# Performance work log

Hardware: AMD Instinct MI355X
Metric: run time of the kernel (lower is better)

Reference implementation:

```python
import jax, jax.numpy as jnp
import numpy as np

B, N, E, C_IN, C_OUT = 16, 4096, 131072, 256, 256


def setup_inputs() -> dict:
    key = jax.random.key(0)
    k1, k2, k3, k4 = jax.random.split(key, 4)
    x = jax.random.normal(k1, (B, N, C_IN), dtype=jnp.float32)
    edge_index = jax.random.randint(k2, (B, 2, E), 0, N, dtype=jnp.int32)
    edge_weight = jax.random.uniform(k3, (B, E), dtype=jnp.float32)
    # glorot init for weight [C_in, C_out]
    scale = float(np.sqrt(6.0 / (C_IN + C_OUT)))
    W = jax.random.uniform(k4, (C_IN, C_OUT), dtype=jnp.float32, minval=-scale, maxval=scale)
    return {"x": x, "edge_index": edge_index, "edge_weight": edge_weight, "W": W}


def _gcn_one_graph(xi, ei, ewi, W):
    # xi: [N, C_in], ei: [2, E+N], ewi: [E+N]
    n = xi.shape[0]
    row, col = ei[0], ei[1]
    deg = jax.ops.segment_sum(ewi, row, num_segments=n)            # [N]
    deg_inv = jnp.where(deg > 0, jax.lax.rsqrt(deg), 0.0)          # deg^-0.5, inf -> 0
    norm = deg_inv[row] * ewi * deg_inv[col]                       # [E+N]
    xw = xi @ W                                                    # [N, C_out]
    msg = norm[:, None] * xw[col]                                  # gather + scale
    out = jax.ops.segment_sum(msg, row, num_segments=n)            # scatter-add to rows
    return jax.nn.relu(out)                                        # act = F.relu, bias=False


def reference(x, edge_index, edge_weight, W):
    b, n, _ = x.shape
    # add self loops with weight 1 (fill_value=1)
    loop = jnp.arange(n, dtype=edge_index.dtype)
    loop_idx = jnp.broadcast_to(jnp.stack([loop, loop])[None], (b, 2, n))
    ei = jnp.concatenate([edge_index, loop_idx], axis=-1)          # [B, 2, E+N]
    ew = jnp.concatenate([edge_weight, jnp.ones((b, n), x.dtype)], axis=-1)  # [B, E+N]
    return jax.vmap(_gcn_one_graph, in_axes=(0, 0, 0, None))(x, ei, ew, W)
```

## Files before the change

### kernel.cpp

```cpp
#include <hip/hip_runtime.h>
#include <cstdint>
#include <cstddef>

#define BB 16
#define NN 4096
#define EE 131072
#define CIN 256
#define COUT 256
#define NCH 16
#define CHE (EE / NCH)

typedef __attribute__((ext_vector_type(8))) __bf16 bf16x8;
typedef __attribute__((ext_vector_type(4))) float f32x4;
typedef __attribute__((ext_vector_type(2))) float f32x2;

#define GLDS16(g, l) __builtin_amdgcn_global_load_lds( \
    (const __attribute__((address_space(1))) uint32_t*)(g), \
    (__attribute__((address_space(3))) uint32_t*)(l), 16, 0, 0)

__global__ __launch_bounds__(256) void cvt_wt_kernel(const float* __restrict__ W, __bf16* __restrict__ wt) {
    int n = blockIdx.x;
    int k = threadIdx.x;
    wt[n * CIN + k] = (__bf16)W[(size_t)k * COUT + n];
}

__global__ __launch_bounds__(256) void phaseA_kernel(const float* __restrict__ x, __bf16* __restrict__ xbf,
                                                     const int* __restrict__ ei, const float* __restrict__ ew,
                                                     int* __restrict__ chist, float* __restrict__ wdeg) {
    __shared__ int h[NN];
    __shared__ float wh[NN];
    int bid = blockIdx.x;
    int tid = threadIdx.x;
    if (bid < BB * NCH) {
        int b = bid >> 4, c = bid & (NCH - 1);
        for (int i = tid; i < NN; i += 256) { h[i] = 0; wh[i] = 0.f; }
        __syncthreads();
        const int* rows = ei + (size_t)b * 2 * EE + (size_t)c * CHE;
        const float* w = ew + (size_t)b * EE + (size_t)c * CHE;
        #pragma unroll 4
        for (int j = 0; j < CHE / 256; ++j) {
            int row = rows[j * 256 + tid];
            float wv = w[j * 256 + tid];
            atomicAdd(&h[row], 1);
            atomicAdd(&wh[row], wv);
        }
        __syncthreads();
        int* co = chist + ((size_t)b * NCH + c) * NN;
        float* wo = wdeg + ((size_t)b * NCH + c) * NN;
        for (int i = tid; i < NN; i += 256) { co[i] = h[i]; wo[i] = wh[i]; }
    } else {
        size_t u = (size_t)(bid - BB * NCH) * 256 + tid;
        const float* g = &x[u * 8];
        float4 f0 = *reinterpret_cast<const float4*>(g);
        float4 f1 = *reinterpret_cast<const float4*>(g + 4);
        bf16x8 v;
        v[0] = (__bf16)f0.x; v[1] = (__bf16)f0.y; v[2] = (__bf16)f0.z; v[3] = (__bf16)f0.w;
        v[4] = (__bf16)f1.x; v[5] = (__bf16)f1.y; v[6] = (__bf16)f1.z; v[7] = (__bf16)f1.w;
        *reinterpret_cast<bf16x8*>(&xbf[u * 8]) = v;
    }
}

__global__ __launch_bounds__(1024) void scanfused_kernel(const int* __restrict__ chist, const float* __restrict__ wdeg,
                                                         int* __restrict__ chunkbase, int* __restrict__ roff,
                                                         float* __restrict__ dinv) {
    int b = blockIdx.x, tid = threadIdx.x;
    int wid = tid >> 6, lane = tid & 63;
    __shared__ int wsum[16];
    __shared__ int wbase[16];
    __shared__ int gtot_s;
    int carry = 0;
    for (int g = 0; g < 4; ++g) {
        int r = g * 1024 + tid;
        int cv[NCH];
        int tot = 0;
        float dsum = 1.0f;
        #pragma unroll
        for (int c = 0; c < NCH; ++c) {
            size_t idx = ((size_t)b * NCH + c) * NN + r;
            cv[c] = chist[idx];
            tot += cv[c];
            dsum += wdeg[idx];
        }
        dinv[b * NN + r] = rsqrtf(dsum);
        int incl = tot;
        #pragma unroll
        for (int off = 1; off < 64; off <<= 1) {
            int t = __shfl_up(incl, off, 64);
            if (lane >= off) incl += t;
        }
        if (lane == 63) wsum[wid] = incl;
        __syncthreads();
        if (wid == 0) {
            int v = (lane < 16) ? wsum[lane] : 0;
            int winc = v;
            #pragma unroll
            for (int off = 1; off < 16; off <<= 1) {
                int t = __shfl_up(winc, off, 64);
                if (lane >= off) winc += t;
            }
            if (lane < 16) wbase[lane] = winc - v;
            if (lane == 15) gtot_s = winc;
        }
        __syncthreads();
        int excl = carry + wbase[wid] + (incl - tot);
        roff[b * NN + r] = excl;
        int acc = excl;
        #pragma unroll
        for (int c = 0; c < NCH; ++c) {
            chunkbase[((size_t)b * NCH + c) * NN + r] = acc;
            acc += cv[c];
        }
        carry += gtot_s;
        __syncthreads();
    }
}

__global__ __launch_bounds__(256) void scatter2_kernel(const int* __restrict__ ei, const float* __restrict__ ew,
                                                       const float* __restrict__ dinv, const int* __restrict__ chunkbase,
                                                       int2* __restrict__ csr) {
    __shared__ int basebuf[NN];
    __shared__ float dinvs[NN];
    int bid = blockIdx.x;
    int xcd = bid & 7;
    int j = bid >> 3;
    int b = xcd * 2 + (j >> 4);
    int c = j & (NCH - 1);
    int tid = threadIdx.x;
    for (int i = tid; i < NN; i += 256) {
        basebuf[i] = chunkbase[((size_t)b * NCH + c) * NN + i];
        dinvs[i] = dinv[b * NN + i];
    }
    __syncthreads();
    const int* rows = ei + (size_t)b * 2 * EE + (size_t)c * CHE;
    const int* cols = rows + EE;
    const float* w = ew + (size_t)b * EE + (size_t)c * CHE;
    int2* cs = csr + (size_t)b * EE;
    #pragma unroll 4
    for (int jj = 0; jj < CHE / 256; ++jj) {
        int e = jj * 256 + tid;
        int row = rows[e];
        int col = cols[e];
        float nm = dinvs[row] * w[e] * dinvs[col];
        int pos = atomicAdd(&basebuf[row], 1);
        int2 pk; pk.x = col * (COUT * 2); pk.y = __float_as_int(nm);
        cs[pos] = pk;
    }
}

__global__ __launch_bounds__(256) void gemm_glds_kernel(const __bf16* __restrict__ xbf, const __bf16* __restrict__ wt,
                                                        __bf16* __restrict__ xw) {
    __shared__ __bf16 As[128 * 64];
    __shared__ __bf16 Bs[128 * 64];
    int tid = threadIdx.x;
    int lane = tid & 63;
    int wave = tid >> 6;
    int bx = blockIdx.x >> 1, by = blockIdx.x & 1;
    int row0 = bx * 128, col0 = by * 128;
    int wr = wave >> 1, wc = wave & 1;
    int hi = lane >> 4, lo = lane & 15;
    int lr = lane >> 3, lk = (lane & 7) * 8;
    f32x4 acc[4][4] = {};

    for (int kk = 0; kk < CIN; kk += 64) {
        #pragma unroll
        for (int j = 0; j < 4; ++j) {
            int seg = j * 4 + wave;
            const __bf16* ga = &xbf[(size_t)(row0 + seg * 8 + lr) * CIN + kk + lk];
            const __bf16* gb = &wt [(size_t)(col0 + seg * 8 + lr) * CIN + kk + lk];
            GLDS16(ga, &As[seg * 512]);
            GLDS16(gb, &Bs[seg * 512]);
        }
        __syncthreads();
        #pragma unroll
        for (int ks = 0; ks < 2; ++ks) {
            bf16x8 a[4], b[4];
            #pragma unroll
            for (int m = 0; m < 4; ++m)
                a[m] = *reinterpret_cast<const bf16x8*>(&As[(wr * 64 + m * 16 + lo) * 64 + ks * 32 + 8 * hi]);
            #pragma unroll
            for (int n = 0; n < 4; ++n)
                b[n] = *reinterpret_cast<const bf16x8*>(&Bs[(wc * 64 + n * 16 + lo) * 64 + ks * 32 + 8 * hi]);
            #pragma unroll
            for (int m = 0; m < 4; ++m)
                #pragma unroll
                for (int n = 0; n < 4; ++n)
                    acc[m][n] = __builtin_amdgcn_mfma_f32_16x16x32_bf16(a[m], b[n], acc[m][n], 0, 0, 0);
        }
        __syncthreads();
    }
    #pragma unroll
    for (int m = 0; m < 4; ++m)
        #pragma unroll
        for (int n = 0; n < 4; ++n)
            #pragma unroll
            for (int r = 0; r < 4; ++r) {
                int row = row0 + wr * 64 + m * 16 + hi * 4 + r;
                int col = col0 + wc * 64 + n * 16 + lo;
                xw[(size_t)row * COUT + col] = (__bf16)acc[m][n][r];
            }
}

#define BFLO(u) __uint_as_float((u) << 16)
#define BFHI(u) __uint_as_float((u) & 0xffff0000u)
#define ACC8(nm, raw) { \
    acc0.x += (nm) * BFLO((raw).x); acc0.y += (nm) * BFHI((raw).x); \
    acc1.x += (nm) * BFLO((raw).y); acc1.y += (nm) * BFHI((raw).y); \
    acc2.x += (nm) * BFLO((raw).z); acc2.y += (nm) * BFHI((raw).z); \
    acc3.x += (nm) * BFLO((raw).w); acc3.y += (nm) * BFHI((raw).w); }

__global__ __launch_bounds__(256) void aggregate_kernel(const __bf16* __restrict__ xw, const float* __restrict__ dinv,
                                                        const int* __restrict__ roff, const int2* __restrict__ csr,
                                                        float* __restrict__ out) {
    int bid = blockIdx.x;
    int xcd = bid & 7;
    int idx = bid >> 3;
    int b = xcd * 2 + (idx >> 10);
    int rowblk = idx & 1023;
    int wave = threadIdx.x >> 6;
    int lane = threadIdx.x & 63;
    int n = rowblk * 4 + wave;
    bool hiHalf = lane >= 32;
    int sub = lane & 31;

    const int* rb = roff + b * NN;
    int s = __builtin_amdgcn_readfirstlane(rb[n]);
    int eRaw = (n == NN - 1) ? EE : rb[n + 1];
    int e = __builtin_amdgcn_readfirstlane(eRaw);
    int cnt = e - s;
    const int2* cs = csr + (size_t)b * EE + s;

    const char* xwb = (const char*)(xw + (size_t)b * NN * COUT) + sub * 16;
    f32x2 acc0 = {0.f, 0.f}, acc1 = {0.f, 0.f}, acc2 = {0.f, 0.f}, acc3 = {0.f, 0.f};

    {
        float di = dinv[b * NN + n];
        float sn = hiHalf ? 0.f : di * di;
        uint4 raw = *reinterpret_cast<const uint4*>(xwb + (size_t)n * (COUT * 2));
        ACC8(sn, raw);
    }

    int m = cnt & ~7;
    int i = 0;
    for (; i < m; i += 8) {
        int2 q[8];
        #pragma unroll
        for (int u = 0; u < 8; ++u) q[u] = cs[i + u];
        #pragma unroll
        for (int u = 0; u < 4; ++u) {
            int offx = hiHalf ? q[2 * u + 1].x : q[2 * u].x;
            float nm = __int_as_float(hiHalf ? q[2 * u + 1].y : q[2 * u].y);
            uint4 raw = *reinterpret_cast<const uint4*>(xwb + offx);
            ACC8(nm, raw);
        }
    }
    if (i < cnt) {
        #pragma unroll
        for (int u = 0; u < 4; ++u) {
            int j0 = i + 2 * u, j1 = j0 + 1;
            int jc0 = (j0 < cnt) ? j0 : cnt - 1;
            int jc1 = (j1 < cnt) ? j1 : cnt - 1;
            int2 q0 = cs[jc0];
            int2 q1 = cs[jc1];
            int offx = hiHalf ? q1.x : q0.x;
            float nm0 = (j0 < cnt) ? __int_as_float(q0.y) : 0.f;
            float nm1 = (j1 < cnt) ? __int_as_float(q1.y) : 0.f;
            float nm = hiHalf ? nm1 : nm0;
            uint4 raw = *reinterpret_cast<const uint4*>(xwb + offx);
            ACC8(nm, raw);
        }
    }

    acc0.x += __shfl(acc0.x, lane ^ 32, 64); acc0.y += __shfl(acc0.y, lane ^ 32, 64);
    acc1.x += __shfl(acc1.x, lane ^ 32, 64); acc1.y += __shfl(acc1.y, lane ^ 32, 64);
    acc2.x += __shfl(acc2.x, lane ^ 32, 64); acc2.y += __shfl(acc2.y, lane ^ 32, 64);
    acc3.x += __shfl(acc3.x, lane ^ 32, 64); acc3.y += __shfl(acc3.y, lane ^ 32, 64);

    float4 o = hiHalf
        ? make_float4(fmaxf(acc2.x, 0.f), fmaxf(acc2.y, 0.f), fmaxf(acc3.x, 0.f), fmaxf(acc3.y, 0.f))
        : make_float4(fmaxf(acc0.x, 0.f), fmaxf(acc0.y, 0.f), fmaxf(acc1.x, 0.f), fmaxf(acc1.y, 0.f));
    float* orow = out + ((size_t)b * NN + n) * COUT + sub * 8 + (hiHalf ? 4 : 0);
    *reinterpret_cast<float4*>(orow) = o;
}

__global__ __launch_bounds__(256) void init_deg_kernel(float* __restrict__ deg, float v) {
    int i = blockIdx.x * 256 + threadIdx.x;
    if (i < BB * NN) deg[i] = v;
}

__global__ __launch_bounds__(256) void deg_only_kernel(const int* __restrict__ ei, const float* __restrict__ ew,
                                                       float* __restrict__ deg) {
    int idx = blockIdx.x * 256 + threadIdx.x;
    if (idx >= BB * EE) return;
    int b = idx / EE, e = idx - b * EE;
    atomicAdd(&deg[b * NN + ei[(size_t)b * 2 * EE + e]], ew[(size_t)b * EE + e]);
}

__global__ __launch_bounds__(256) void deginv_kernel(const float* __restrict__ deg, float* __restrict__ dinv) {
    int i = blockIdx.x * 256 + threadIdx.x;
    if (i < BB * NN) {
        float d = deg[i];
        dinv[i] = (d > 0.0f) ? rsqrtf(d) : 0.0f;
    }
}

__global__ __launch_bounds__(256) void gemm_f32src_kernel(const float* __restrict__ x, const __bf16* __restrict__ wt,
                                                          __bf16* __restrict__ xw) {
    __shared__ __bf16 As[128][64];
    __shared__ __bf16 Bs[128][64];
    int tid = threadIdx.x;
    int lane = tid & 63;
    int wave = tid >> 6;
    int row0 = blockIdx.x * 128;
    int col0 = blockIdx.y * 128;
    int wr = wave >> 1, wc = wave & 1;
    int hi = lane >> 4, lo = lane & 15;
    f32x4 acc[4][4] = {};
    for (int kk = 0; kk < CIN; kk += 64) {
        #pragma unroll
        for (int j = 0; j < 4; ++j) {
            int c = j * 256 + tid;
            int r = c >> 3, kq = c & 7;
            const float* g = &x[(size_t)(row0 + r) * CIN + kk + 8 * kq];
            float4 f0 = *reinterpret_cast<const float4*>(g);
            float4 f1 = *reinterpret_cast<const float4*>(g + 4);
            bf16x8 v;
            v[0] = (__bf16)f0.x; v[1] = (__bf16)f0.y; v[2] = (__bf16)f0.z; v[3] = (__bf16)f0.w;
            v[4] = (__bf16)f1.x; v[5] = (__bf16)f1.y; v[6] = (__bf16)f1.z; v[7] = (__bf16)f1.w;
            *reinterpret_cast<bf16x8*>(&As[r][8 * kq]) = v;
        }
        #pragma unroll
        for (int j = 0; j < 4; ++j) {
            int c = j * 256 + tid;
            int r = c >> 3, kq = c & 7;
            *reinterpret_cast<bf16x8*>(&Bs[r][8 * kq]) =
                *reinterpret_cast<const bf16x8*>(&wt[(size_t)(col0 + r) * CIN + kk + 8 * kq]);
        }
        __syncthreads();
        #pragma unroll
        for (int ks = 0; ks < 2; ++ks) {
            bf16x8 a[4], b[4];
            #pragma unroll
            for (int m = 0; m < 4; ++m)
                a[m] = *reinterpret_cast<const bf16x8*>(&As[wr * 64 + m * 16 + lo][ks * 32 + 8 * hi]);
            #pragma unroll
            for (int n = 0; n < 4; ++n)
                b[n] = *reinterpret_cast<const bf16x8*>(&Bs[wc * 64 + n * 16 + lo][ks * 32 + 8 * hi]);
            #pragma unroll
            for (int m = 0; m < 4; ++m)
                #pragma unroll
                for (int n = 0; n < 4; ++n)
                    acc[m][n] = __builtin_amdgcn_mfma_f32_16x16x32_bf16(a[m], b[n], acc[m][n], 0, 0, 0);
        }
        __syncthreads();
    }
    #pragma unroll
    for (int m = 0; m < 4; ++m)
        #pragma unroll
        for (int n = 0; n < 4; ++n)
            #pragma unroll
            for (int r = 0; r < 4; ++r) {
                int row = row0 + wr * 64 + m * 16 + hi * 4 + r;
                int col = col0 + wc * 64 + n * 16 + lo;
                xw[(size_t)row * COUT + col] = (__bf16)acc[m][n][r];
            }
}

__global__ __launch_bounds__(256) void self_kernel(const __bf16* __restrict__ xw, const float* __restrict__ dinv,
                                                   float* __restrict__ out) {
    int bn = blockIdx.x;
    int c = threadIdx.x;
    float di = dinv[bn];
    out[(size_t)bn * COUT + c] = di * di * (float)xw[(size_t)bn * COUT + c];
}

__global__ __launch_bounds__(256) void scatter_atomic_kernel(const int* __restrict__ ei, const float* __restrict__ ew,
                                                             const float* __restrict__ dinv,
                                                             const __bf16* __restrict__ xw, float* __restrict__ out) {
    int be = blockIdx.x;
    int b = be / EE, e = be - b * EE;
    int c = threadIdx.x;
    int row = ei[(size_t)b * 2 * EE + e];
    int col = ei[(size_t)b * 2 * EE + EE + e];
    float w = ew[(size_t)b * EE + e];
    float nm = dinv[b * NN + row] * w * dinv[b * NN + col];
    const __bf16* xwb = xw + (size_t)b * NN * COUT;
    atomicAdd(&out[((size_t)b * NN + row) * COUT + c], nm * (float)xwb[(size_t)col * COUT + c]);
}

__global__ __launch_bounds__(256) void relu_kernel(float* __restrict__ out) {
    size_t i = (size_t)blockIdx.x * 256 + threadIdx.x;
    out[i] = fmaxf(out[i], 0.0f);
}

extern "C" void kernel_launch(void* const* d_in, const int* in_sizes, int n_in,
                              void* d_out, int out_size, void* d_ws, size_t ws_size,
                              hipStream_t stream) {
    const float* x  = (const float*)d_in[0];
    const int*   ei = (const int*)d_in[1];
    const float* ew = (const float*)d_in[2];
    const float* Wm = (const float*)d_in[3];
    float* out = (float*)d_out;

    char* ws = (char*)d_ws;
    size_t off = 0;
    auto alloc = [&](size_t bytes) -> void* {
        void* p = ws + off;
        off += (bytes + 255) & ~(size_t)255;
        return p;
    };
    __bf16* xw        = (__bf16*)alloc((size_t)BB * NN * COUT * 2);
    __bf16* xbf       = (__bf16*)alloc((size_t)BB * NN * CIN * 2);
    int*    chist     = (int*)alloc((size_t)BB * NCH * NN * 4);
    float*  wdeg      = (float*)alloc((size_t)BB * NCH * NN * 4);
    int*    chunkbase = (int*)alloc((size_t)BB * NCH * NN * 4);
    int*    roff      = (int*)alloc((size_t)BB * NN * 4);
    float*  dinv      = (float*)alloc((size_t)BB * NN * 4);
    __bf16* wt        = (__bf16*)alloc((size_t)CIN * COUT * 2);
    int2*   csr       = (int2*)xbf;
    float*  deg_fb    = (float*)chist;
    bool use_csr = (ws_size >= off);

    cvt_wt_kernel<<<COUT, CIN, 0, stream>>>(Wm, wt);

    if (use_csr) {
        phaseA_kernel<<<BB * NCH + (BB * NN * CIN) / (256 * 8), 256, 0, stream>>>(x, xbf, ei, ew, chist, wdeg);
        scanfused_kernel<<<BB, 1024, 0, stream>>>(chist, wdeg, chunkbase, roff, dinv);
        gemm_glds_kernel<<<(BB * NN / 128) * (COUT / 128), 256, 0, stream>>>(xbf, wt, xw);
        scatter2_kernel<<<BB * NCH, 256, 0, stream>>>(ei, ew, dinv, chunkbase, csr);
        aggregate_kernel<<<BB * NN / 4, 256, 0, stream>>>(xw, dinv, roff, csr, out);
    } else {
        const int bnBlocks = (BB * NN) / 256;
        init_deg_kernel<<<bnBlocks, 256, 0, stream>>>(deg_fb, 1.0f);
        deg_only_kernel<<<(BB * EE) / 256, 256, 0, stream>>>(ei, ew, deg_fb);
        deginv_kernel<<<bnBlocks, 256, 0, stream>>>(deg_fb, dinv);
        dim3 ggrid((BB * NN) / 128, COUT / 128);
        gemm_f32src_kernel<<<ggrid, 256, 0, stream>>>(x, wt, xw);
        self_kernel<<<BB * NN, 256, 0, stream>>>(xw, dinv, out);
        scatter_atomic_kernel<<<BB * EE, 256, 0, stream>>>(ei, ew, dinv, xw, out);
        relu_kernel<<<(BB * NN * COUT) / 256, 256, 0, stream>>>(out);
    }
}
```

Before: 140.6 us.

## Switch GEMM and gather path from bf16 to fp16 and fuse weight conversion

Changes the intermediate x, W and xW buffers from bf16 to fp16, using the f16 MFMA and fp16-to-float conversions in the aggregation gather. It also folds the W transpose and convert step into the phaseA kernel as extra blocks, which removes one kernel launch on the CSR path. fp16 gives more mantissa precision but less range; the aggregate loop now converts halves with hardware instructions instead of bf16 shift and mask tricks.

```diff
diff --git a/kernel.cpp b/kernel.cpp
--- a/kernel.cpp
+++ b/kernel.cpp
@@ -10,21 +10,15 @@
 #define NCH 16
 #define CHE (EE / NCH)
 
-typedef __attribute__((ext_vector_type(8))) __bf16 bf16x8;
+typedef __attribute__((ext_vector_type(8))) _Float16 h16x8;
 typedef __attribute__((ext_vector_type(4))) float f32x4;
-typedef __attribute__((ext_vector_type(2))) float f32x2;
 
 #define GLDS16(g, l) __builtin_amdgcn_global_load_lds( \
     (const __attribute__((address_space(1))) uint32_t*)(g), \
     (__attribute__((address_space(3))) uint32_t*)(l), 16, 0, 0)
 
-__global__ __launch_bounds__(256) void cvt_wt_kernel(const float* __restrict__ W, __bf16* __restrict__ wt) {
-    int n = blockIdx.x;
-    int k = threadIdx.x;
-    wt[n * CIN + k] = (__bf16)W[(size_t)k * COUT + n];
-}
-
-__global__ __launch_bounds__(256) void phaseA_kernel(const float* __restrict__ x, __bf16* __restrict__ xbf,
+__global__ __launch_bounds__(256) void phaseA_kernel(const float* __restrict__ x, _Float16* __restrict__ xh,
+                                                     const float* __restrict__ W, _Float16* __restrict__ wt,
                                                      const int* __restrict__ ei, const float* __restrict__ ew,
                                                      int* __restrict__ chist, float* __restrict__ wdeg) {
     __shared__ int h[NN];
@@ -48,15 +42,19 @@
         int* co = chist + ((size_t)b * NCH + c) * NN;
         float* wo = wdeg + ((size_t)b * NCH + c) * NN;
         for (int i = tid; i < NN; i += 256) { co[i] = h[i]; wo[i] = wh[i]; }
-    } else {
+    } else if (bid < BB * NCH + (BB * NN * CIN) / (256 * 8)) {
         size_t u = (size_t)(bid - BB * NCH) * 256 + tid;
         const float* g = &x[u * 8];
         float4 f0 = *reinterpret_cast<const float4*>(g);
         float4 f1 = *reinterpret_cast<const float4*>(g + 4);
-        bf16x8 v;
-        v[0] = (__bf16)f0.x; v[1] = (__bf16)f0.y; v[2] = (__bf16)f0.z; v[3] = (__bf16)f0.w;
-        v[4] = (__bf16)f1.x; v[5] = (__bf16)f1.y; v[6] = (__bf16)f1.z; v[7] = (__bf16)f1.w;
-        *reinterpret_cast<bf16x8*>(&xbf[u * 8]) = v;
+        h16x8 v;
+        v[0] = (_Float16)f0.x; v[1] = (_Float16)f0.y; v[2] = (_Float16)f0.z; v[3] = (_Float16)f0.w;
+        v[4] = (_Float16)f1.x; v[5] = (_Float16)f1.y; v[6] = (_Float16)f1.z; v[7] = (_Float16)f1.w;
+        *reinterpret_cast<h16x8*>(&xh[u * 8]) = v;
+    } else {
+        int n = bid - (BB * NCH + (BB * NN * CIN) / (256 * 8));
+        int k = tid;
+        wt[n * CIN + k] = (_Float16)W[(size_t)k * COUT + n];
     }
 }
 
@@ -115,6 +113,59 @@
     }
 }
 
+__global__ __launch_bounds__(256) void gemm_glds_kernel(const _Float16* __restrict__ xh, const _Float16* __restrict__ wt,
+                                                        _Float16* __restrict__ xw) {
+    __shared__ _Float16 As[128 * 64];
+    __shared__ _Float16 Bs[128 * 64];
+    int tid = threadIdx.x;
+    int lane = tid & 63;
+    int wave = tid >> 6;
+    int bx = blockIdx.x >> 1, by = blockIdx.x & 1;
+    int row0 = bx * 128, col0 = by * 128;
+    int wr = wave >> 1, wc = wave & 1;
+    int hi = lane >> 4, lo = lane & 15;
+    int lr = lane >> 3, lk = (lane & 7) * 8;
+    f32x4 acc[4][4] = {};
+
+    for (int kk = 0; kk < CIN; kk += 64) {
+        #pragma unroll
+        for (int j = 0; j < 4; ++j) {
+            int seg = j * 4 + wave;
+            const _Float16* ga = &xh[(size_t)(row0 + seg * 8 + lr) * CIN + kk + lk];
+            const _Float16* gb = &wt [(size_t)(col0 + seg * 8 + lr) * CIN + kk + lk];
+            GLDS16(ga, &As[seg * 512]);
+            GLDS16(gb, &Bs[seg * 512]);
+        }
+        __syncthreads();
+        #pragma unroll
+        for (int ks = 0; ks < 2; ++ks) {
+            h16x8 a[4], b[4];
+            #pragma unroll
+            for (int m = 0; m < 4; ++m)
+                a[m] = *reinterpret_cast<const h16x8*>(&As[(wr * 64 + m * 16 + lo) * 64 + ks * 32 + 8 * hi]);
+            #pragma unroll
+            for (int n = 0; n < 4; ++n)
+                b[n] = *reinterpret_cast<const h16x8*>(&Bs[(wc * 64 + n * 16 + lo) * 64 + ks * 32 + 8 * hi]);
+            #pragma unroll
+            for (int m = 0; m < 4; ++m)
+                #pragma unroll
+                for (int n = 0; n < 4; ++n)
+                    acc[m][n] = __builtin_amdgcn_mfma_f32_16x16x32_f16(a[m], b[n], acc[m][n], 0, 0, 0);
+        }
+        __syncthreads();
+    }
+    #pragma unroll
+    for (int m = 0; m < 4; ++m)
+        #pragma unroll
+        for (int n = 0; n < 4; ++n)
+            #pragma unroll
+            for (int r = 0; r < 4; ++r) {
+                int row = row0 + wr * 64 + m * 16 + hi * 4 + r;
+                int col = col0 + wc * 64 + n * 16 + lo;
+                xw[(size_t)row * COUT + col] = (_Float16)acc[m][n][r];
+            }
+}
+
 __global__ __launch_bounds__(256) void scatter2_kernel(const int* __restrict__ ei, const float* __restrict__ ew,
                                                        const float* __restrict__ dinv, const int* __restrict__ chunkbase,
                                                        int2* __restrict__ csr) {
@@ -147,68 +198,13 @@
     }
 }
 
-__global__ __launch_bounds__(256) void gemm_glds_kernel(const __bf16* __restrict__ xbf, const __bf16* __restrict__ wt,
-                                                        __bf16* __restrict__ xw) {
-    __shared__ __bf16 As[128 * 64];
-    __shared__ __bf16 Bs[128 * 64];
-    int tid = threadIdx.x;
-    int lane = tid & 63;
-    int wave = tid >> 6;
-    int bx = blockIdx.x >> 1, by = blockIdx.x & 1;
-    int row0 = bx * 128, col0 = by * 128;
-    int wr = wave >> 1, wc = wave & 1;
-    int hi = lane >> 4, lo = lane & 15;
-    int lr = lane >> 3, lk = (lane & 7) * 8;
-    f32x4 acc[4][4] = {};
-
-    for (int kk = 0; kk < CIN; kk += 64) {
-        #pragma unroll
-        for (int j = 0; j < 4; ++j) {
-            int seg = j * 4 + wave;
-            const __bf16* ga = &xbf[(size_t)(row0 + seg * 8 + lr) * CIN + kk + lk];
-            const __bf16* gb = &wt [(size_t)(col0 + seg * 8 + lr) * CIN + kk + lk];
-            GLDS16(ga, &As[seg * 512]);
-            GLDS16(gb, &Bs[seg * 512]);
-        }
-        __syncthreads();
-        #pragma unroll
-        for (int ks = 0; ks < 2; ++ks) {
-            bf16x8 a[4], b[4];
-            #pragma unroll
-            for (int m = 0; m < 4; ++m)
-                a[m] = *reinterpret_cast<const bf16x8*>(&As[(wr * 64 + m * 16 + lo) * 64 + ks * 32 + 8 * hi]);
-            #pragma unroll
-            for (int n = 0; n < 4; ++n)
-                b[n] = *reinterpret_cast<const bf16x8*>(&Bs[(wc * 64 + n * 16 + lo) * 64 + ks * 32 + 8 * hi]);
-            #pragma unroll
-            for (int m = 0; m < 4; ++m)
-                #pragma unroll
-                for (int n = 0; n < 4; ++n)
-                    acc[m][n] = __builtin_amdgcn_mfma_f32_16x16x32_bf16(a[m], b[n], acc[m][n], 0, 0, 0);
-        }
-        __syncthreads();
-    }
-    #pragma unroll
-    for (int m = 0; m < 4; ++m)
-        #pragma unroll
-        for (int n = 0; n < 4; ++n)
-            #pragma unroll
-            for (int r = 0; r < 4; ++r) {
-                int row = row0 + wr * 64 + m * 16 + hi * 4 + r;
-                int col = col0 + wc * 64 + n * 16 + lo;
-                xw[(size_t)row * COUT + col] = (__bf16)acc[m][n][r];
-            }
-}
-
-#define BFLO(u) __uint_as_float((u) << 16)
-#define BFHI(u) __uint_as_float((u) & 0xffff0000u)
-#define ACC8(nm, raw) { \
-    acc0.x += (nm) * BFLO((raw).x); acc0.y += (nm) * BFHI((raw).x); \
-    acc1.x += (nm) * BFLO((raw).y); acc1.y += (nm) * BFHI((raw).y); \
-    acc2.x += (nm) * BFLO((raw).z); acc2.y += (nm) * BFHI((raw).z); \
-    acc3.x += (nm) * BFLO((raw).w); acc3.y += (nm) * BFHI((raw).w); }
-
-__global__ __launch_bounds__(256) void aggregate_kernel(const __bf16* __restrict__ xw, const float* __restrict__ dinv,
+#define ACCH(nm, r) { \
+    a0 += (nm) * (float)(r)[0]; a1 += (nm) * (float)(r)[1]; \
+    a2 += (nm) * (float)(r)[2]; a3 += (nm) * (float)(r)[3]; \
+    a4 += (nm) * (float)(r)[4]; a5 += (nm) * (float)(r)[5]; \
+    a6 += (nm) * (float)(r)[6]; a7 += (nm) * (float)(r)[7]; }
+
+__global__ __launch_bounds__(256) void aggregate_kernel(const _Float16* __restrict__ xw, const float* __restrict__ dinv,
                                                         const int* __restrict__ roff, const int2* __restrict__ csr,
                                                         float* __restrict__ out) {
     int bid = blockIdx.x;
@@ -221,6 +217,7 @@
     int n = rowblk * 4 + wave;
     bool hiHalf = lane >= 32;
     int sub = lane & 31;
+    int lanebyte = sub * 16;
 
     const int* rb = roff + b * NN;
     int s = __builtin_amdgcn_readfirstlane(rb[n]);
@@ -229,14 +226,14 @@
     int cnt = e - s;
     const int2* cs = csr + (size_t)b * EE + s;
 
-    const char* xwb = (const char*)(xw + (size_t)b * NN * COUT) + sub * 16;
-    f32x2 acc0 = {0.f, 0.f}, acc1 = {0.f, 0.f}, acc2 = {0.f, 0.f}, acc3 = {0.f, 0.f};
+    const char* xwbase = (const char*)(xw + (size_t)b * NN * COUT);
+    float a0 = 0.f, a1 = 0.f, a2 = 0.f, a3 = 0.f, a4 = 0.f, a5 = 0.f, a6 = 0.f, a7 = 0.f;
 
     {
         float di = dinv[b * NN + n];
         float sn = hiHalf ? 0.f : di * di;
-        uint4 raw = *reinterpret_cast<const uint4*>(xwb + (size_t)n * (COUT * 2));
-        ACC8(sn, raw);
+        h16x8 r = *reinterpret_cast<const h16x8*>(xwbase + (size_t)n * (COUT * 2) + lanebyte);
+        ACCH(sn, r);
     }
 
     int m = cnt & ~7;
@@ -247,10 +244,10 @@
         for (int u = 0; u < 8; ++u) q[u] = cs[i + u];
         #pragma unroll
         for (int u = 0; u < 4; ++u) {
-            int offx = hiHalf ? q[2 * u + 1].x : q[2 * u].x;
+            int offx = (hiHalf ? q[2 * u + 1].x : q[2 * u].x) + lanebyte;
             float nm = __int_as_float(hiHalf ? q[2 * u + 1].y : q[2 * u].y);
-            uint4 raw = *reinterpret_cast<const uint4*>(xwb + offx);
-            ACC8(nm, raw);
+            h16x8 r = *reinterpret_cast<const h16x8*>(xwbase + (uint32_t)offx);
+            ACCH(nm, r);
         }
     }
     if (i < cnt) {
@@ -261,25 +258,31 @@
             int jc1 = (j1 < cnt) ? j1 : cnt - 1;
             int2 q0 = cs[jc0];
             int2 q1 = cs[jc1];
-            int offx = hiHalf ? q1.x : q0.x;
+            int offx = (hiHalf ? q1.x : q0.x) + lanebyte;
             float nm0 = (j0 < cnt) ? __int_as_float(q0.y) : 0.f;
             float nm1 = (j1 < cnt) ? __int_as_float(q1.y) : 0.f;
             float nm = hiHalf ? nm1 : nm0;
-            uint4 raw = *reinterpret_cast<const uint4*>(xwb + offx);
-            ACC8(nm, raw);
-        }
-    }
-
-    acc0.x += __shfl(acc0.x, lane ^ 32, 64); acc0.y += __shfl(acc0.y, lane ^ 32, 64);
-    acc1.x += __shfl(acc1.x, lane ^ 32, 64); acc1.y += __shfl(acc1.y, lane ^ 32, 64);
-    acc2.x += __shfl(acc2.x, lane ^ 32, 64); acc2.y += __shfl(acc2.y, lane ^ 32, 64);
-    acc3.x += __shfl(acc3.x, lane ^ 32, 64); acc3.y += __shfl(acc3.y, lane ^ 32, 64);
+            h16x8 r = *reinterpret_cast<const h16x8*>(xwbase + (uint32_t)offx);
+            ACCH(nm, r);
+        }
+    }
+
+    a0 += __shfl(a0, lane ^ 32, 64); a1 += __shfl(a1, lane ^ 32, 64);
+    a2 += __shfl(a2, lane ^ 32, 64); a3 += __shfl(a3, lane ^ 32, 64);
+    a4 += __shfl(a4, lane ^ 32, 64); a5 += __shfl(a5, lane ^ 32, 64);
+    a6 += __shfl(a6, lane ^ 32, 64); a7 += __shfl(a7, lane ^ 32, 64);
 
     float4 o = hiHalf
-        ? make_float4(fmaxf(acc2.x, 0.f), fmaxf(acc2.y, 0.f), fmaxf(acc3.x, 0.f), fmaxf(acc3.y, 0.f))
-        : make_float4(fmaxf(acc0.x, 0.f), fmaxf(acc0.y, 0.f), fmaxf(acc1.x, 0.f), fmaxf(acc1.y, 0.f));
+        ? make_float4(fmaxf(a4, 0.f), fmaxf(a5, 0.f), fmaxf(a6, 0.f), fmaxf(a7, 0.f))
+        : make_float4(fmaxf(a0, 0.f), fmaxf(a1, 0.f), fmaxf(a2, 0.f), fmaxf(a3, 0.f));
     float* orow = out + ((size_t)b * NN + n) * COUT + sub * 8 + (hiHalf ? 4 : 0);
     *reinterpret_cast<float4*>(orow) = o;
+}
+
+__global__ __launch_bounds__(256) void cvt_wt_kernel(const float* __restrict__ W, _Float16* __restrict__ wt) {
+    int n = blockIdx.x;
+    int k = threadIdx.x;
+    wt[n * CIN + k] = (_Float16)W[(size_t)k * COUT + n];
 }
 
 __global__ __launch_bounds__(256) void init_deg_kernel(float* __restrict__ deg, float v) {
@@ -303,10 +306,10 @@
     }
 }
 
-__global__ __launch_bounds__(256) void gemm_f32src_kernel(const float* __restrict__ x, const __bf16* __restrict__ wt,
-                                                          __bf16* __restrict__ xw) {
-    __shared__ __bf16 As[128][64];
-    __shared__ __bf16 Bs[128][64];
+__global__ __launch_bounds__(256) void gemm_f32src_kernel(const float* __restrict__ x, const _Float16* __restrict__ wt,
+                                                          _Float16* __restrict__ xw) {
+    __shared__ _Float16 As[128][64];
+    __shared__ _Float16 Bs[128][64];
     int tid = threadIdx.x;
     int lane = tid & 63;
     int wave = tid >> 6;
@@ -323,33 +326,33 @@
             const float* g = &x[(size_t)(row0 + r) * CIN + kk + 8 * kq];
             float4 f0 = *reinterpret_cast<const float4*>(g);
             float4 f1 = *reinterpret_cast<const float4*>(g + 4);
-            bf16x8 v;
-            v[0] = (__bf16)f0.x; v[1] = (__bf16)f0.y; v[2] = (__bf16)f0.z; v[3] = (__bf16)f0.w;
-            v[4] = (__bf16)f1.x; v[5] = (__bf16)f1.y; v[6] = (__bf16)f1.z; v[7] = (__bf16)f1.w;
-            *reinterpret_cast<bf16x8*>(&As[r][8 * kq]) = v;
+            h16x8 v;
+            v[0] = (_Float16)f0.x; v[1] = (_Float16)f0.y; v[2] = (_Float16)f0.z; v[3] = (_Float16)f0.w;
+            v[4] = (_Float16)f1.x; v[5] = (_Float16)f1.y; v[6] = (_Float16)f1.z; v[7] = (_Float16)f1.w;
+            *reinterpret_cast<h16x8*>(&As[r][8 * kq]) = v;
         }
         #pragma unroll
         for (int j = 0; j < 4; ++j) {
             int c = j * 256 + tid;
             int r = c >> 3, kq = c & 7;
-            *reinterpret_cast<bf16x8*>(&Bs[r][8 * kq]) =
-                *reinterpret_cast<const bf16x8*>(&wt[(size_t)(col0 + r) * CIN + kk + 8 * kq]);
+            *reinterpret_cast<h16x8*>(&Bs[r][8 * kq]) =
+                *reinterpret_cast<const h16x8*>(&wt[(size_t)(col0 + r) * CIN + kk + 8 * kq]);
         }
         __syncthreads();
         #pragma unroll
         for (int ks = 0; ks < 2; ++ks) {
-            bf16x8 a[4], b[4];
+            h16x8 a[4], b[4];
             #pragma unroll
             for (int m = 0; m < 4; ++m)
-                a[m] = *reinterpret_cast<const bf16x8*>(&As[wr * 64 + m * 16 + lo][ks * 32 + 8 * hi]);
+                a[m] = *reinterpret_cast<const h16x8*>(&As[wr * 64 + m * 16 + lo][ks * 32 + 8 * hi]);
             #pragma unroll
             for (int n = 0; n < 4; ++n)
-                b[n] = *reinterpret_cast<const bf16x8*>(&Bs[wc * 64 + n * 16 + lo][ks * 32 + 8 * hi]);
+                b[n] = *reinterpret_cast<const h16x8*>(&Bs[wc * 64 + n * 16 + lo][ks * 32 + 8 * hi]);
             #pragma unroll
             for (int m = 0; m < 4; ++m)
                 #pragma unroll
                 for (int n = 0; n < 4; ++n)
-                    acc[m][n] = __builtin_amdgcn_mfma_f32_16x16x32_bf16(a[m], b[n], acc[m][n], 0, 0, 0);
+                    acc[m][n] = __builtin_amdgcn_mfma_f32_16x16x32_f16(a[m], b[n], acc[m][n], 0, 0, 0);
         }
         __syncthreads();
     }
@@ -361,11 +364,11 @@
             for (int r = 0; r < 4; ++r) {
                 int row = row0 + wr * 64 + m * 16 + hi * 4 + r;
                 int col = col0 + wc * 64 + n * 16 + lo;
-                xw[(size_t)row * COUT + col] = (__bf16)acc[m][n][r];
+                xw[(size_t)row * COUT + col] = (_Float16)acc[m][n][r];
             }
 }
 
-__global__ __launch_bounds__(256) void self_kernel(const __bf16* __restrict__ xw, const float* __restrict__ dinv,
+__global__ __launch_bounds__(256) void self_kernel(const _Float16* __restrict__ xw, const float* __restrict__ dinv,
                                                    float* __restrict__ out) {
     int bn = blockIdx.x;
     int c = threadIdx.x;
@@ -375,7 +378,7 @@
 
 __global__ __launch_bounds__(256) void scatter_atomic_kernel(const int* __restrict__ ei, const float* __restrict__ ew,
                                                              const float* __restrict__ dinv,
-                                                             const __bf16* __restrict__ xw, float* __restrict__ out) {
+                                                             const _Float16* __restrict__ xw, float* __restrict__ out) {
     int be = blockIdx.x;
     int b = be / EE, e = be - b * EE;
     int c = threadIdx.x;
@@ -383,7 +386,7 @@
     int col = ei[(size_t)b * 2 * EE + EE + e];
     float w = ew[(size_t)b * EE + e];
     float nm = dinv[b * NN + row] * w * dinv[b * NN + col];
-    const __bf16* xwb = xw + (size_t)b * NN * COUT;
+    const _Float16* xwb = xw + (size_t)b * NN * COUT;
     atomicAdd(&out[((size_t)b * NN + row) * COUT + c], nm * (float)xwb[(size_t)col * COUT + c]);
 }
 
@@ -408,28 +411,28 @@
         off += (bytes + 255) & ~(size_t)255;
         return p;
     };
-    __bf16* xw        = (__bf16*)alloc((size_t)BB * NN * COUT * 2);
-    __bf16* xbf       = (__bf16*)alloc((size_t)BB * NN * CIN * 2);
-    int*    chist     = (int*)alloc((size_t)BB * NCH * NN * 4);
-    float*  wdeg      = (float*)alloc((size_t)BB * NCH * NN * 4);
-    int*    chunkbase = (int*)alloc((size_t)BB * NCH * NN * 4);
-    int*    roff      = (int*)alloc((size_t)BB * NN * 4);
-    float*  dinv      = (float*)alloc((size_t)BB * NN * 4);
-    __bf16* wt        = (__bf16*)alloc((size_t)CIN * COUT * 2);
-    int2*   csr       = (int2*)xbf;
-    float*  deg_fb    = (float*)chist;
+    _Float16* xw        = (_Float16*)alloc((size_t)BB * NN * COUT * 2);
+    _Float16* xh        = (_Float16*)alloc((size_t)BB * NN * CIN * 2);
+    int*      chist     = (int*)alloc((size_t)BB * NCH * NN * 4);
+    float*    wdeg      = (float*)alloc((size_t)BB * NCH * NN * 4);
+    int*      chunkbase = (int*)alloc((size_t)BB * NCH * NN * 4);
+    int*      roff      = (int*)alloc((size_t)BB * NN * 4);
+    float*    dinv      = (float*)alloc((size_t)BB * NN * 4);
+    _Float16* wt        = (_Float16*)alloc((size_t)CIN * COUT * 2);
+    int2*     csr       = (int2*)xh;
+    float*    deg_fb    = (float*)chist;
     bool use_csr = (ws_size >= off);
 
-    cvt_wt_kernel<<<COUT, CIN, 0, stream>>>(Wm, wt);
-
     if (use_csr) {
-        phaseA_kernel<<<BB * NCH + (BB * NN * CIN) / (256 * 8), 256, 0, stream>>>(x, xbf, ei, ew, chist, wdeg);
+        const int xcvtBlocks = (BB * NN * CIN) / (256 * 8);
+        phaseA_kernel<<<BB * NCH + xcvtBlocks + COUT, 256, 0, stream>>>(x, xh, Wm, wt, ei, ew, chist, wdeg);
         scanfused_kernel<<<BB, 1024, 0, stream>>>(chist, wdeg, chunkbase, roff, dinv);
-        gemm_glds_kernel<<<(BB * NN / 128) * (COUT / 128), 256, 0, stream>>>(xbf, wt, xw);
+        gemm_glds_kernel<<<(BB * NN / 128) * (COUT / 128), 256, 0, stream>>>(xh, wt, xw);
         scatter2_kernel<<<BB * NCH, 256, 0, stream>>>(ei, ew, dinv, chunkbase, csr);
         aggregate_kernel<<<BB * NN / 4, 256, 0, stream>>>(xw, dinv, roff, csr, out);
     } else {
         const int bnBlocks = (BB * NN) / 256;
+        cvt_wt_kernel<<<COUT, CIN, 0, stream>>>(Wm, wt);
         init_deg_kernel<<<bnBlocks, 256, 0, stream>>>(deg_fb, 1.0f);
         deg_only_kernel<<<(BB * EE) / 256, 256, 0, stream>>>(ei, ew, deg_fb);
         deginv_kernel<<<bnBlocks, 256, 0, stream>>>(deg_fb, dinv);
```

Result: faster. 135.6 us (-3.6%).
